# Performance work log

Hardware: AMD Instinct MI355X
Metric: run time of the kernel (lower is better)

## Reference

```python
import jax, jax.numpy as jnp
import numpy as np

NUM_NODES = 50000
NUM_EDGES = 800000
IN_C = 64
OUT_C = 64


def setup_inputs() -> dict:
    key = jax.random.key(0)
    k1, k2, k3, k4 = jax.random.split(key, 4)
    x = jax.random.normal(k1, (NUM_NODES, IN_C), dtype=jnp.float32)
    edge_index = jax.random.randint(k2, (2, NUM_EDGES), 0, NUM_NODES, dtype=jnp.int64)
    # nn.Linear params (kaiming-uniform-ish init scale)
    lim = 1.0 / np.sqrt(IN_C)
    W = jax.random.uniform(k3, (OUT_C, IN_C), minval=-lim, maxval=lim, dtype=jnp.float32)
    b = jax.random.uniform(k4, (OUT_C,), minval=-lim, maxval=lim, dtype=jnp.float32)
    return {"x": x, "edge_index": edge_index, "W": W, "b": b}


def reference(x, edge_index, W, b):
    num_nodes = x.shape[0]
    src = edge_index[0]
    tgt = edge_index[1]
    # Stage 1: degree of target nodes via scatter-add of ones
    deg = jax.ops.segment_sum(jnp.ones(src.shape[0], dtype=jnp.float32), tgt,
                              num_segments=num_nodes)
    deg_inv_sqrt = jnp.clip(deg, 1.0, None) ** -0.5  # [N]
    # Stage 2-3: gather source features, scale by norm_src * norm_tgt
    norm = deg_inv_sqrt[src] * deg_inv_sqrt[tgt]       # [E]
    messages = x[src] * norm[:, None]                  # [E, C]
    # Stage 4: scatter-add aggregation into target nodes
    agg = jax.ops.segment_sum(messages, tgt, num_segments=num_nodes)  # [N, C]
    # Stage 5-6: linear + relu
    out = agg @ W.T + b
    return jax.nn.relu(out)
```

## Files before the change

kernel.cpp:

```cpp
#include <hip/hip_runtime.h>
#include <hip/hip_fp16.h>

#define NN 50000
#define NE 800000
#define NC 64
#define CAP 64
#define NXCD 8
#define NODES_PER (NN / NXCD)
#define BIN_BLOCKS 2048

__global__ void FusedGCN_zero_kernel(int4* __restrict__ p, int n4) {
    int t = blockIdx.x * blockDim.x + threadIdx.x;
    if (t < n4) p[t] = make_int4(0, 0, 0, 0);
}


__global__ __launch_bounds__(256) void FusedGCN_binA2_kernel(
        const int* __restrict__ src,
        const int* __restrict__ tgt,
        int* __restrict__ counters,
        unsigned short* __restrict__ binned) {
    int grp = blockIdx.x & (NXCD - 1);
    int sub = blockIdx.x >> 3;
    int lo = grp * NODES_PER, hi = lo + NODES_PER;
    const int stride = (BIN_BLOCKS / NXCD) * 256;
    for (int e = sub * 256 + threadIdx.x; e < NE; e += stride) {
        int t = tgt[e];
        if (t >= lo && t < hi) {
            int pos = atomicAdd(&counters[t], 1);
            if (pos < CAP) binned[(t << 6) + pos] = (unsigned short)src[e];
        }
    }
}

__global__ void FusedGCN_xscaleH_kernel(const float4* __restrict__ x4,
                                        const int* __restrict__ counters,
                                        uint2* __restrict__ xsh2) {
    int t = blockIdx.x * blockDim.x + threadIdx.x;
    if (t < (NN + 1) * (NC / 4)) {
        int row = t >> 4;
        float4 v = make_float4(0.f, 0.f, 0.f, 0.f);
        if (row < NN) {
            float d = rsqrtf(fmaxf((float)counters[row], 1.0f));
            v = x4[t];
            v.x *= d; v.y *= d; v.z *= d; v.w *= d;
        }
        __half2 h0 = __floats2half2_rn(v.x, v.y);
        __half2 h1 = __floats2half2_rn(v.z, v.w);
        uint2 u;
        u.x = *(unsigned int*)&h0;
        u.y = *(unsigned int*)&h1;
        xsh2[t] = u;
    }
}

__global__ __launch_bounds__(256) void FusedGCN_aggA_kernel(
        const uint2* __restrict__ xs2,
        const unsigned short* __restrict__ binned,
        const int* __restrict__ counters,
        const float* __restrict__ W,
        const float4* __restrict__ bias4,
        float4* __restrict__ out4) {
    __shared__ float Wt[64][68];
    int tid = threadIdx.x;
    for (int i = tid; i < 64 * 64; i += 256) Wt[i & 63][i >> 6] = W[i];
    __syncthreads();

    int lane = tid & 63;
    int g    = lane >> 4;
    int gl   = lane & 15;
    int node = (blockIdx.x << 4) + ((tid >> 6) << 2) + g;

    int cnt = min(counters[node], CAP);
    ushort4 sv = ((const ushort4*)(binned + ((size_t)node << 6)))[gl];
    int sx = sv.x, sy = sv.y, sz = sv.z, sw = sv.w;

    float4 acc = make_float4(0.f, 0.f, 0.f, 0.f);
    int base = g << 4;

#define H4ACC(raw)                                                   \
    {                                                                \
        __half2 _h0 = *(__half2*)&(raw).x;                           \
        __half2 _h1 = *(__half2*)&(raw).y;                           \
        float2 _f0 = __half22float2(_h0);                            \
        float2 _f1 = __half22float2(_h1);                            \
        acc.x += _f0.x; acc.y += _f0.y;                              \
        acc.z += _f1.x; acc.w += _f1.y;                              \
    }

    for (int q = 0; q < 16; q += 2) {
        int j = q << 2;
        if (j >= cnt) break;
        int L0 = base + q, L1 = base + q + 1;
        int a0 = __shfl(sx, L0), a1 = __shfl(sy, L0);
        int a2 = __shfl(sz, L0), a3 = __shfl(sw, L0);
        int b0 = __shfl(sx, L1), b1 = __shfl(sy, L1);
        int b2 = __shfl(sz, L1), b3 = __shfl(sw, L1);
        int s0 = (j + 0 < cnt) ? a0 : NN, s1 = (j + 1 < cnt) ? a1 : NN;
        int s2 = (j + 2 < cnt) ? a2 : NN, s3 = (j + 3 < cnt) ? a3 : NN;
        int s4 = (j + 4 < cnt) ? b0 : NN, s5 = (j + 5 < cnt) ? b1 : NN;
        int s6 = (j + 6 < cnt) ? b2 : NN, s7 = (j + 7 < cnt) ? b3 : NN;
        uint2 r0 = xs2[(s0 << 4) + gl], r1 = xs2[(s1 << 4) + gl];
        uint2 r2 = xs2[(s2 << 4) + gl], r3 = xs2[(s3 << 4) + gl];
        uint2 r4 = xs2[(s4 << 4) + gl], r5 = xs2[(s5 << 4) + gl];
        uint2 r6 = xs2[(s6 << 4) + gl], r7 = xs2[(s7 << 4) + gl];
        H4ACC(r0) H4ACC(r1) H4ACC(r2) H4ACC(r3)
        H4ACC(r4) H4ACC(r5) H4ACC(r6) H4ACC(r7)
    }
#undef H4ACC

    float dn = rsqrtf(fmaxf((float)cnt, 1.0f));
    acc.x *= dn; acc.y *= dn; acc.z *= dn; acc.w *= dn;

    float4 r = bias4[gl];
#pragma unroll
    for (int k = 0; k < 64; ++k) {
        float ak = __shfl((k & 3) == 0 ? acc.x :
                          (k & 3) == 1 ? acc.y :
                          (k & 3) == 2 ? acc.z : acc.w,
                          base + (k >> 2));
        const float4 w = *(const float4*)&Wt[k][gl << 2];
        r.x = fmaf(ak, w.x, r.x);
        r.y = fmaf(ak, w.y, r.y);
        r.z = fmaf(ak, w.z, r.z);
        r.w = fmaf(ak, w.w, r.w);
    }
    r.x = fmaxf(r.x, 0.f); r.y = fmaxf(r.y, 0.f);
    r.z = fmaxf(r.z, 0.f); r.w = fmaxf(r.w, 0.f);
    out4[(node << 4) + gl] = r;
}

__global__ void FusedGCN_count_kernel(const int* __restrict__ tgt,
                                      int* __restrict__ counters) {
    int e = blockIdx.x * blockDim.x + threadIdx.x;
    if (e < NE) atomicAdd(&counters[tgt[e]], 1);
}

__global__ __launch_bounds__(256) void FusedGCN_alloc_kernel(
        const int* __restrict__ counters,
        int* __restrict__ gcursor,
        int* __restrict__ offsets,
        int* __restrict__ cursor,
        float* __restrict__ dis) {
    int i = blockIdx.x * blockDim.x + threadIdx.x;
    int lane = threadIdx.x & 63;
    int c = (i < NN) ? counters[i] : 0;
    int v = c;
#pragma unroll
    for (int o = 1; o < 64; o <<= 1) {
        int t = __shfl_up(v, o, 64);
        if (lane >= o) v += t;
    }
    int waveTotal = __shfl(v, 63, 64);
    int base = 0;
    if (lane == 63) base = atomicAdd(gcursor, waveTotal);
    base = __shfl(base, 63, 64);
    if (i < NN) {
        int start = base + v - c;
        offsets[i] = start;
        cursor[i]  = start;
        dis[i] = rsqrtf(fmaxf((float)c, 1.0f));
    }
}

__global__ void FusedGCN_bin_kernel(const int* __restrict__ src,
                                    const int* __restrict__ tgt,
                                    int* __restrict__ cursor,
                                    int* __restrict__ binned) {
    int e = blockIdx.x * blockDim.x + threadIdx.x;
    if (e < NE) {
        int pos = atomicAdd(&cursor[tgt[e]], 1);
        binned[pos] = src[e];
    }
}

__global__ __launch_bounds__(256) void FusedGCN_agg_kernel(
        const float* __restrict__ x,
        const int* __restrict__ binned,
        const int* __restrict__ offsets,
        const int* __restrict__ counters,
        const float* __restrict__ dis,
        const float* __restrict__ W,
        const float* __restrict__ bias,
        float* __restrict__ out) {
    __shared__ float Wt[64][65];
    int tid = threadIdx.x;
    for (int i = tid; i < 64 * 64; i += 256) Wt[i & 63][i >> 6] = W[i];
    __syncthreads();

    int lane = tid & 63;
    int node = blockIdx.x * 4 + (tid >> 6);
    if (node >= NN) return;

    int off = offsets[node];
    int end = off + counters[node];
    float acc = 0.0f;
    for (int c = off; c < end; c += 64) {
        int m = min(64, end - c);
        int   sidx = 0;
        float nv   = 0.0f;
        if (lane < m) {
            sidx = binned[c + lane];
            nv   = dis[sidx];
        }
        int j = 0;
        for (; j + 4 <= m; j += 4) {
            int   s0 = __shfl(sidx, j),     s1 = __shfl(sidx, j + 1);
            int   s2 = __shfl(sidx, j + 2), s3 = __shfl(sidx, j + 3);
            float n0 = __shfl(nv, j),       n1 = __shfl(nv, j + 1);
            float n2 = __shfl(nv, j + 2),   n3 = __shfl(nv, j + 3);
            acc = fmaf(x[s0 * NC + lane], n0, acc);
            acc = fmaf(x[s1 * NC + lane], n1, acc);
            acc = fmaf(x[s2 * NC + lane], n2, acc);
            acc = fmaf(x[s3 * NC + lane], n3, acc);
        }
        for (; j < m; ++j) {
            acc = fmaf(x[__shfl(sidx, j) * NC + lane], __shfl(nv, j), acc);
        }
    }
    acc *= dis[node];

    float r = bias[lane];
#pragma unroll
    for (int k = 0; k < 64; ++k) r = fmaf(__shfl(acc, k), Wt[k][lane], r);
    out[node * NC + lane] = fmaxf(r, 0.0f);
}

extern "C" void kernel_launch(void* const* d_in, const int* in_sizes, int n_in,
                              void* d_out, int out_size, void* d_ws, size_t ws_size,
                              hipStream_t stream) {
    const float* x   = (const float*)d_in[0];
    const int*   ei  = (const int*)d_in[1];
    const float* W   = (const float*)d_in[2];
    const float* b   = (const float*)d_in[3];
    const int*   src = ei;
    const int*   tgt = ei + NE;
    float* out = (float*)d_out;

    size_t needA = (size_t)NN * 4 + (size_t)NN * CAP * 2 + (size_t)(NN + 1) * NC * 2;

    if (ws_size >= needA) {
        int*            counters = (int*)d_ws;
        unsigned short* binned   = (unsigned short*)(counters + NN);
        uint2*          xsh2     = (uint2*)((char*)d_ws + (size_t)NN * 4
                                            + (size_t)NN * CAP * 2);

        FusedGCN_zero_kernel<<<(NN / 4 + 255) / 256, 256, 0, stream>>>(
            (int4*)counters, NN / 4);
        FusedGCN_binA2_kernel<<<BIN_BLOCKS, 256, 0, stream>>>(
            src, tgt, counters, binned);
        FusedGCN_xscaleH_kernel<<<((NN + 1) * (NC / 4) + 255) / 256, 256, 0, stream>>>(
            (const float4*)x, counters, xsh2);
        FusedGCN_aggA_kernel<<<NN / 16, 256, 0, stream>>>(
            xsh2, binned, counters, W, (const float4*)b, (float4*)out);
    } else {
        int*   counters = (int*)d_ws;
        int*   gcursor  = counters + NN;
        int*   offsets  = gcursor + 1;
        int*   cursor   = offsets + NN;
        float* dis      = (float*)(cursor + NN);
        int*   binned   = (int*)(dis + NN);

        FusedGCN_zero_kernel<<<(NN / 4 + 255) / 256, 256, 0, stream>>>(
            (int4*)counters, NN / 4);
        hipMemsetAsync(gcursor, 0, sizeof(int), stream);
        FusedGCN_count_kernel<<<(NE + 255) / 256, 256, 0, stream>>>(tgt, counters);
        FusedGCN_alloc_kernel<<<(NN + 255) / 256, 256, 0, stream>>>(
            counters, gcursor, offsets, cursor, dis);
        FusedGCN_bin_kernel<<<(NE + 255) / 256, 256, 0, stream>>>(
            src, tgt, cursor, binned);
        FusedGCN_agg_kernel<<<(NN + 3) / 4, 256, 0, stream>>>(
            x, binned, offsets, counters, dis, W, b, out);
    }
}
```

Baseline: 82.93 us.

## Pre-partition edges into per-XCD buckets before binning

Measured after the change: 123.7 us. 1.49x slower.

```diff
diff --git a/kernel.cpp b/kernel.cpp
--- a/kernel.cpp
+++ b/kernel.cpp
@@ -7,7 +7,11 @@
 #define CAP 64
 #define NXCD 8
 #define NODES_PER (NN / NXCD)
-#define BIN_BLOCKS 2048
+#define PART_BLOCKS 128
+#define EPB (NE / PART_BLOCKS)
+#define BUCKET_CAP 140000
+#define BIN2_BLOCKS 2048
+#define SENTINEL 0xFFFFFFFFu
 
 __global__ void FusedGCN_zero_kernel(int4* __restrict__ p, int n4) {
     int t = blockIdx.x * blockDim.x + threadIdx.x;
@@ -15,21 +19,86 @@
 }
 
 
-__global__ __launch_bounds__(256) void FusedGCN_binA2_kernel(
+__global__ __launch_bounds__(256) void FusedGCN_part_kernel(
         const int* __restrict__ src,
         const int* __restrict__ tgt,
+        int* __restrict__ bcur,
+        unsigned int* __restrict__ buckets) {
+    __shared__ unsigned int buf[NXCD][512];
+    __shared__ int bcnt[NXCD];
+    __shared__ int sbase[NXCD];
+    int tid = threadIdx.x;
+    if (tid < NXCD) bcnt[tid] = 0;
+    __syncthreads();
+
+    int e0 = blockIdx.x * EPB;
+    int e1 = e0 + EPB;
+    for (int base = e0; base < e1; base += 256) {
+        int e = base + tid;
+        if (e < e1) {
+            int t = tgt[e];
+            int s = src[e];
+            int b = t / NODES_PER;
+            unsigned int pk = ((unsigned int)(t - b * NODES_PER) << 16)
+                              | (unsigned int)s;
+            int pos = atomicAdd(&bcnt[b], 1);
+            buf[b][pos] = pk;
+        }
+        __syncthreads();
+        if (tid < NXCD)
+            sbase[tid] = (bcnt[tid] >= 256) ? atomicAdd(&bcur[tid], 256) : -1;
+        __syncthreads();
+#pragma unroll
+        for (int b = 0; b < NXCD; ++b) {
+            int sb = sbase[b];
+            if (sb >= 0 && sb + 256 <= BUCKET_CAP)
+                buckets[(size_t)b * BUCKET_CAP + sb + tid] = buf[b][tid];
+        }
+        __syncthreads();
+#pragma unroll
+        for (int b = 0; b < NXCD; ++b) {
+            if (sbase[b] >= 0) {
+                int mv = bcnt[b] - 256;
+                if (tid < mv) buf[b][tid] = buf[b][256 + tid];
+            }
+        }
+        __syncthreads();
+        if (tid < NXCD && sbase[tid] >= 0) bcnt[tid] -= 256;
+        __syncthreads();
+    }
+#pragma unroll
+    for (int b = 0; b < NXCD; ++b)
+        if (tid >= bcnt[b]) buf[b][tid] = SENTINEL;
+    __syncthreads();
+    if (tid < NXCD)
+        sbase[tid] = (bcnt[tid] > 0) ? atomicAdd(&bcur[tid], 256) : -1;
+    __syncthreads();
+#pragma unroll
+    for (int b = 0; b < NXCD; ++b) {
+        int sb = sbase[b];
+        if (sb >= 0 && sb + 256 <= BUCKET_CAP)
+            buckets[(size_t)b * BUCKET_CAP + sb + tid] = buf[b][tid];
+    }
+}
+
+__global__ __launch_bounds__(256) void FusedGCN_bin3_kernel(
+        const unsigned int* __restrict__ buckets,
+        const int* __restrict__ bcur,
         int* __restrict__ counters,
         unsigned short* __restrict__ binned) {
     int grp = blockIdx.x & (NXCD - 1);
     int sub = blockIdx.x >> 3;
-    int lo = grp * NODES_PER, hi = lo + NODES_PER;
-    const int stride = (BIN_BLOCKS / NXCD) * 256;
-    for (int e = sub * 256 + threadIdx.x; e < NE; e += stride) {
-        int t = tgt[e];
-        if (t >= lo && t < hi) {
-            int pos = atomicAdd(&counters[t], 1);
-            if (pos < CAP) binned[(t << 6) + pos] = (unsigned short)src[e];
-        }
+    int n = bcur[grp];
+    if (n > BUCKET_CAP) n = BUCKET_CAP;
+    const unsigned int* bk = buckets + (size_t)grp * BUCKET_CAP;
+    const int stride = (BIN2_BLOCKS / NXCD) * 256;
+    for (int i = sub * 256 + threadIdx.x; i < n; i += stride) {
+        unsigned int u = bk[i];
+        unsigned int tl = u >> 16;
+        if (tl >= NODES_PER) continue;
+        int t = grp * NODES_PER + (int)tl;
+        int pos = atomicAdd(&counters[t], 1);
+        if (pos < CAP) binned[(t << 6) + pos] = (unsigned short)(u & 0xFFFFu);
     }
 }
 
@@ -237,18 +306,24 @@
     const int*   tgt = ei + NE;
     float* out = (float*)d_out;
 
-    size_t needA = (size_t)NN * 4 + (size_t)NN * CAP * 2 + (size_t)(NN + 1) * NC * 2;
+    size_t off_binned  = (size_t)(NN + NXCD) * 4;
+    size_t off_xs      = off_binned + (size_t)NN * CAP * 2;
+    size_t off_buckets = off_xs + (size_t)(NN + 1) * NC * 2;
+    size_t needA       = off_buckets + (size_t)NXCD * BUCKET_CAP * 4;
 
     if (ws_size >= needA) {
         int*            counters = (int*)d_ws;
-        unsigned short* binned   = (unsigned short*)(counters + NN);
-        uint2*          xsh2     = (uint2*)((char*)d_ws + (size_t)NN * 4
-                                            + (size_t)NN * CAP * 2);
-
-        FusedGCN_zero_kernel<<<(NN / 4 + 255) / 256, 256, 0, stream>>>(
-            (int4*)counters, NN / 4);
-        FusedGCN_binA2_kernel<<<BIN_BLOCKS, 256, 0, stream>>>(
-            src, tgt, counters, binned);
+        int*            bcur     = counters + NN;
+        unsigned short* binned   = (unsigned short*)((char*)d_ws + off_binned);
+        uint2*          xsh2     = (uint2*)((char*)d_ws + off_xs);
+        unsigned int*   buckets  = (unsigned int*)((char*)d_ws + off_buckets);
+
+        FusedGCN_zero_kernel<<<((NN + NXCD) / 4 + 255) / 256, 256, 0, stream>>>(
+            (int4*)counters, (NN + NXCD) / 4);
+        FusedGCN_part_kernel<<<PART_BLOCKS, 256, 0, stream>>>(
+            src, tgt, bcur, buckets);
+        FusedGCN_bin3_kernel<<<BIN2_BLOCKS, 256, 0, stream>>>(
+            buckets, bcur, counters, binned);
         FusedGCN_xscaleH_kernel<<<((NN + 1) * (NC / 4) + 255) / 256, 256, 0, stream>>>(
             (const float4*)x, counters, xsh2);
         FusedGCN_aggA_kernel<<<NN / 16, 256, 0, stream>>>(
```
